# Performance work log

Hardware: AMD Instinct MI355X
Metric: run time of the kernel (lower is better)

Reference implementation:

```python
import jax, jax.numpy as jnp
import numpy as np

N_NODES = 50000
N_EDGES = 800000
IN_F, HID, OUT_F = 256, 128, 64
ATTN_SLOPE = 0.2   # DGL GATConv negative_slope default
ACT_SLOPE = 0.01   # nn.LeakyReLU default


def setup_inputs() -> dict:
    key = jax.random.key(0)
    ks = jax.random.split(key, 7)
    x = jax.random.normal(ks[0], (N_NODES, IN_F), dtype=jnp.float32)
    src = jax.random.randint(ks[1], (N_EDGES,), 0, N_NODES, dtype=jnp.int32)
    dst = jax.random.randint(ks[2], (N_EDGES,), 0, N_NODES, dtype=jnp.int32)
    W_gat = jax.random.normal(ks[3], (IN_F, HID), dtype=jnp.float32) * (1.0 / np.sqrt(IN_F))
    attn_l = jax.random.normal(ks[4], (HID,), dtype=jnp.float32) * 0.1
    attn_r = jax.random.normal(ks[5], (HID,), dtype=jnp.float32) * 0.1
    bias_gat = jnp.zeros((HID,), dtype=jnp.float32)
    W_lin = jax.random.normal(ks[6], (OUT_F, HID), dtype=jnp.float32) * (1.0 / np.sqrt(HID))
    return {"x": x, "src": src, "dst": dst, "W_gat": W_gat, "attn_l": attn_l,
            "attn_r": attn_r, "bias_gat": bias_gat, "W_lin": W_lin}


def reference(x, src, dst, W_gat, attn_l, attn_r, bias_gat, W_lin):
    N = x.shape[0]
    # GATConv (num_heads=1): linear projection then additive attention
    feat = x @ W_gat                         # [N, HID]
    el = feat @ attn_l                        # [N]  (sum(feat * a_l, -1))
    er = feat @ attn_r                        # [N]
    # per-edge logits, leaky_relu(0.2)
    e = jax.nn.leaky_relu(el[src] + er[dst], negative_slope=ATTN_SLOPE)  # [E]
    # segment softmax over edges grouped by destination node
    e_max = jax.ops.segment_max(e, dst, num_segments=N)  # [N] (-inf for isolated)
    alpha = jnp.exp(e - e_max[dst])                      # [E]
    denom = jax.ops.segment_sum(alpha, dst, num_segments=N)
    a = alpha / denom[dst]                               # [E]
    # scatter-weighted aggregation of source features
    msg = a[:, None] * feat[src]                         # [E, HID]
    agg = jax.ops.segment_sum(msg, dst, num_segments=N) + bias_gat  # [N, HID]
    # outer wrapper: LeakyReLU(0.01), squeeze (head dim already gone), linear no bias
    gene = jax.nn.leaky_relu(agg, negative_slope=ACT_SLOPE)
    return gene @ W_lin.T                                # [N, OUT_F]
```

## Files before the change

kernel.cpp:

```cpp
#include <hip/hip_runtime.h>
#include <hip/hip_bf16.h>


#define NNODES 50000
#define NEDGES 800000
#define IN_F   256
#define HID    128
#define OUTF   64

#define PA_EPT   12
#define PA_EDGES (256 * PA_EPT)
#define PA_NB    ((NEDGES + PA_EDGES - 1) / PA_EDGES)
#define NBKT     ((NNODES + 255) / 256)
#define BCAP     5120
#define GB       ((NNODES / 16 + 7) / 8)

typedef unsigned short u16;
typedef unsigned long long u64;
typedef __bf16 bf16x8 __attribute__((ext_vector_type(8)));
typedef float  f32x4  __attribute__((ext_vector_type(4)));

__device__ __forceinline__ u16 f2b(float f) {
    union { float f; unsigned u; } v; v.f = f;
    unsigned u = v.u;
    return (u16)((u + 0x7fffu + ((u >> 16) & 1u)) >> 16);
}
__device__ __forceinline__ float b2f_lo(unsigned v) {
    union { unsigned u; float f; } c; c.u = (v & 0xffffu) << 16; return c.f;
}
__device__ __forceinline__ float b2f_hi(unsigned v) {
    union { unsigned u; float f; } c; c.u = v & 0xffff0000u; return c.f;
}
__device__ __forceinline__ float lrelu02_exp(float t) {
    t = t > 0.f ? t : 0.2f * t;
    return __expf(t);
}

__global__ __launch_bounds__(256) void pack0(const float* __restrict__ Wg,
                                             const float* __restrict__ Wl,
                                             u16* __restrict__ pWg,
                                             u16* __restrict__ pWl,
                                             int* __restrict__ bcnt) {
    int blk = blockIdx.x, tid = threadIdx.x;
    if (blk < 16) {
        int t = blk * 256 + tid;
        int lane = t & 63, tile = t >> 6;
        int nt = tile & 7, kt = tile >> 3;
        int col = lane & 15, quad = lane >> 4;
        int krow = kt * 32 + quad * 8;
        int ncol = nt * 16 + col;
#pragma unroll
        for (int j = 0; j < 8; j++) pWg[t * 8 + j] = f2b(Wg[(krow + j) * HID + ncol]);
    } else if (blk < 20) {
        int t = (blk - 16) * 256 + tid;
        int lane = t & 63, tile = t >> 6;
        int nt = tile & 3, kt = tile >> 2;
        int col = lane & 15, quad = lane >> 4;
        int o  = nt * 16 + col;
        int k0 = kt * 32 + quad * 8;
#pragma unroll
        for (int j = 0; j < 8; j++) pWl[t * 8 + j] = f2b(Wl[o * HID + k0 + j]);
    } else {
        if (tid < NBKT) bcnt[tid] = 0;
    }
}

__global__ __launch_bounds__(256) void k_mega(
        const float* __restrict__ x, const u16* __restrict__ pWg,
        const float* __restrict__ al_, const float* __restrict__ ar_,
        unsigned* __restrict__ feat2, float* __restrict__ el, float* __restrict__ er,
        const int* __restrict__ src, const int* __restrict__ dst,
        int* __restrict__ bcnt, u64* __restrict__ pairs) {
    __shared__ char smem[35840];
    int blk = blockIdx.x, tid = threadIdx.x;

    if (blk < GB) {
        int wave = tid >> 6, lane = tid & 63;
        int strip0 = blk * 8 + wave * 2;
        if (strip0 >= NNODES / 16) return;
        bool two = (strip0 + 1 < NNODES / 16);
        int mA = strip0 * 16, mB = mA + 16;
        int col = lane & 15, quad = lane >> 4;

        f32x4 accA[8] = {}, accB[8] = {};
        const float* xrA = x + (size_t)(mA + col) * IN_F + quad * 8;
        const float* xrB = x + (size_t)(mB + col) * IN_F + quad * 8;
#pragma unroll
        for (int kt = 0; kt < 8; kt++) {
            f32x4 a0 = *reinterpret_cast<const f32x4*>(xrA + kt * 32);
            f32x4 a1 = *reinterpret_cast<const f32x4*>(xrA + kt * 32 + 4);
            f32x4 b0 = {}, b1 = {};
            if (two) {
                b0 = *reinterpret_cast<const f32x4*>(xrB + kt * 32);
                b1 = *reinterpret_cast<const f32x4*>(xrB + kt * 32 + 4);
            }
            bf16x8 avA, avB;
#pragma unroll
            for (int j = 0; j < 4; j++) {
                avA[j] = (__bf16)a0[j]; avA[4 + j] = (__bf16)a1[j];
                avB[j] = (__bf16)b0[j]; avB[4 + j] = (__bf16)b1[j];
            }
#pragma unroll
            for (int nt = 0; nt < 8; nt++) {
                bf16x8 b = *reinterpret_cast<const bf16x8*>(pWg + ((kt * 8 + nt) * 64 + lane) * 8);
                accA[nt] = __builtin_amdgcn_mfma_f32_16x16x32_bf16(avA, b, accA[nt], 0, 0, 0);
                accB[nt] = __builtin_amdgcn_mfma_f32_16x16x32_bf16(avB, b, accB[nt], 0, 0, 0);
            }
        }
        for (int ss = 0; ss < 2; ss++) {
            if (ss == 1 && !two) break;
            f32x4* acc = ss ? accB : accA;
            int m0 = ss ? mB : mA;
            float pl[4] = {0, 0, 0, 0}, pr[4] = {0, 0, 0, 0};
#pragma unroll
            for (int nt = 0; nt < 8; nt++) {
                float alv = al_[nt * 16 + col], arv = ar_[nt * 16 + col];
#pragma unroll
                for (int reg = 0; reg < 4; reg++) {
                    pl[reg] += acc[nt][reg] * alv;
                    pr[reg] += acc[nt][reg] * arv;
                }
            }
#pragma unroll
            for (int m = 1; m < 16; m <<= 1)
#pragma unroll
                for (int reg = 0; reg < 4; reg++) {
                    pl[reg] += __shfl_xor(pl[reg], m, 64);
                    pr[reg] += __shfl_xor(pr[reg], m, 64);
                }
            if (col == 0) {
#pragma unroll
                for (int reg = 0; reg < 4; reg++) {
                    el[m0 + quad * 4 + reg] = pl[reg];
                    er[m0 + quad * 4 + reg] = pr[reg];
                }
            }
#pragma unroll
            for (int nt = 0; nt < 8; nt++)
#pragma unroll
                for (int reg = 0; reg < 4; reg++) {
                    u16* fp = (u16*)feat2;
                    fp[(size_t)(m0 + quad * 4 + reg) * HID + nt * 16 + col] = f2b(acc[nt][reg]);
                }
        }
        return;
    }

    int* hist    = (int*)smem;
    int* binbase = hist + 256;
    int* gbase   = binbase + 256;
    int* fill    = gbase + 256;
    int* stmp    = fill + 256;
    u64* spair   = (u64*)(smem + 8192);
    unsigned char* sbin = (unsigned char*)(smem + 8192 + 24576);

    int e0 = (blk - GB) * PA_EDGES;
    int cnt = NEDGES - e0; if (cnt > PA_EDGES) cnt = PA_EDGES;

    hist[tid] = 0; fill[tid] = 0;
    __syncthreads();

    int es[PA_EPT], ed[PA_EPT];
#pragma unroll
    for (int j = 0; j < PA_EPT; j++) {
        int idx = e0 + j * 256 + tid;
        if (idx < NEDGES) {
            es[j] = src[idx];
            ed[j] = dst[idx];
            atomicAdd(&hist[ed[j] >> 8], 1);
        } else ed[j] = -1;
    }
    __syncthreads();

    stmp[tid] = (tid < NBKT) ? hist[tid] : 0;
    __syncthreads();
#pragma unroll
    for (int ofs = 1; ofs < 256; ofs <<= 1) {
        int u = (tid >= ofs) ? stmp[tid - ofs] : 0;
        __syncthreads();
        stmp[tid] += u;
        __syncthreads();
    }
    if (tid < NBKT) {
        binbase[tid] = stmp[tid] - hist[tid];
        if (hist[tid] > 0)
            gbase[tid] = tid * BCAP + atomicAdd(&bcnt[tid], hist[tid]);
    }
    __syncthreads();

#pragma unroll
    for (int j = 0; j < PA_EPT; j++) {
        if (ed[j] >= 0) {
            int b = ed[j] >> 8;
            int r = atomicAdd(&fill[b], 1);
            int loc = binbase[b] + r;
            spair[loc] = ((u64)(unsigned)ed[j] << 32) | (unsigned)es[j];
            sbin[loc] = (unsigned char)b;
        }
    }
    __syncthreads();

    for (int i = tid; i < cnt; i += 256) {
        int b = sbin[i];
        pairs[gbase[b] + (i - binbase[b])] = spair[i];
    }
}

__global__ __launch_bounds__(512) void k_fine(const u64* __restrict__ pairs,
                                              const int* __restrict__ bcnt,
                                              const float* __restrict__ el,
                                              const float* __restrict__ er,
                                              int* __restrict__ rowptr,
                                              int* __restrict__ esrc,
                                              float* __restrict__ ew,
                                              float* __restrict__ den) {
    __shared__ int sbc[256];
    __shared__ int nh[256];
    __shared__ int wsum[256];
    __shared__ int cur[256];
    __shared__ float dls[256];
    __shared__ float erl[256];

    int b = blockIdx.x, tid = threadIdx.x;
    int nb = b << 8;
    int nn = NNODES - nb; if (nn > 256) nn = 256;

    if (tid < 256) sbc[tid] = (tid < NBKT) ? bcnt[tid] : 0;
    __syncthreads();
#pragma unroll
    for (int ofs = 1; ofs < 256; ofs <<= 1) {
        int u = 0;
        if (tid < 256 && tid >= ofs) u = sbc[tid - ofs];
        __syncthreads();
        if (tid < 256) sbc[tid] += u;
        __syncthreads();
    }
    int cntb = bcnt[b];
    int base = sbc[b] - cntb;
    const u64* reg = pairs + (size_t)b * BCAP;

    if (tid < 256) {
        nh[tid] = 0;
        dls[tid] = 0.f;
        erl[tid] = (tid < nn) ? er[nb + tid] : 0.f;
    }
    __syncthreads();
    for (int i = tid; i < cntb; i += 512) {
        int d = (int)(unsigned)(reg[i] >> 32);
        atomicAdd(&nh[d - nb], 1);
    }
    __syncthreads();

    int c = (tid < 256) ? nh[tid] : 0;
    if (tid < 256) wsum[tid] = c;
    __syncthreads();
#pragma unroll
    for (int ofs = 1; ofs < 256; ofs <<= 1) {
        int u = 0;
        if (tid < 256 && tid >= ofs) u = wsum[tid - ofs];
        __syncthreads();
        if (tid < 256) wsum[tid] += u;
        __syncthreads();
    }
    if (tid < 256) {
        int o = base + wsum[tid] - c;
        cur[tid] = o;
        if (tid < nn) rowptr[nb + tid] = o;
    }
    if (b == NBKT - 1 && tid == 0) rowptr[NNODES] = NEDGES;
    __syncthreads();

    for (int i = tid; i < cntb; i += 512) {
        u64 p = reg[i];
        int s_ = (int)(unsigned)(p & 0xffffffffu);
        int d  = (int)(unsigned)(p >> 32);
        int dl = d - nb;
        float w = lrelu02_exp(el[s_] + erl[dl]);
        int pos = atomicAdd(&cur[dl], 1);
        esrc[pos] = s_;
        ew[pos] = w;
        atomicAdd(&dls[dl], w);
    }
    __syncthreads();
    if (tid < nn) den[nb + tid] = dls[tid];
}

__global__ __launch_bounds__(256) void k_aggout(const int* __restrict__ rowptr,
                                                const int* __restrict__ esrc,
                                                const float* __restrict__ ew,
                                                const float* __restrict__ den,
                                                const unsigned* __restrict__ feat2,
                                                const float* __restrict__ bias,
                                                const u16* __restrict__ pWl,
                                                float* __restrict__ out) {
    __shared__ unsigned sg[16 * 68];
    int wave = threadIdx.x >> 6, lane = threadIdx.x & 63;
    int m0 = blockIdx.x * 16;
    float bl = bias[lane * 2 + 0], bh = bias[lane * 2 + 1];

    for (int i = 0; i < 4; i++) {
        int r = wave * 4 + i;
        int n = m0 + r;
        int beg = rowptr[n], end = rowptr[n + 1];

        float p0 = 0.f, p1 = 0.f, q0 = 0.f, q1 = 0.f;
        float r0 = 0.f, r1 = 0.f, t0 = 0.f, t1 = 0.f;
        float u0 = 0.f, u1 = 0.f, x0 = 0.f, x1 = 0.f;
        float y0 = 0.f, y1 = 0.f, z0 = 0.f, z1 = 0.f;
        int j = beg;
        for (; j + 8 <= end; j += 8) {
            int s0 = esrc[j],     s1 = esrc[j + 1], s2 = esrc[j + 2], s3 = esrc[j + 3];
            int s4 = esrc[j + 4], s5 = esrc[j + 5], s6 = esrc[j + 6], s7 = esrc[j + 7];
            unsigned v0 = feat2[(size_t)s0 * 64 + lane];
            unsigned v1 = feat2[(size_t)s1 * 64 + lane];
            unsigned v2 = feat2[(size_t)s2 * 64 + lane];
            unsigned v3 = feat2[(size_t)s3 * 64 + lane];
            unsigned v4 = feat2[(size_t)s4 * 64 + lane];
            unsigned v5 = feat2[(size_t)s5 * 64 + lane];
            unsigned v6 = feat2[(size_t)s6 * 64 + lane];
            unsigned v7 = feat2[(size_t)s7 * 64 + lane];
            float w0 = ew[j],     w1 = ew[j + 1], w2 = ew[j + 2], w3 = ew[j + 3];
            float w4 = ew[j + 4], w5 = ew[j + 5], w6 = ew[j + 6], w7 = ew[j + 7];
            p0 += w0 * b2f_lo(v0); p1 += w0 * b2f_hi(v0);
            q0 += w1 * b2f_lo(v1); q1 += w1 * b2f_hi(v1);
            r0 += w2 * b2f_lo(v2); r1 += w2 * b2f_hi(v2);
            t0 += w3 * b2f_lo(v3); t1 += w3 * b2f_hi(v3);
            u0 += w4 * b2f_lo(v4); u1 += w4 * b2f_hi(v4);
            x0 += w5 * b2f_lo(v5); x1 += w5 * b2f_hi(v5);
            y0 += w6 * b2f_lo(v6); y1 += w6 * b2f_hi(v6);
            z0 += w7 * b2f_lo(v7); z1 += w7 * b2f_hi(v7);
        }
        if (j + 4 <= end) {
            int s0 = esrc[j], s1 = esrc[j + 1], s2 = esrc[j + 2], s3 = esrc[j + 3];
            unsigned v0 = feat2[(size_t)s0 * 64 + lane];
            unsigned v1 = feat2[(size_t)s1 * 64 + lane];
            unsigned v2 = feat2[(size_t)s2 * 64 + lane];
            unsigned v3 = feat2[(size_t)s3 * 64 + lane];
            float w0 = ew[j], w1 = ew[j + 1], w2 = ew[j + 2], w3 = ew[j + 3];
            p0 += w0 * b2f_lo(v0); p1 += w0 * b2f_hi(v0);
            q0 += w1 * b2f_lo(v1); q1 += w1 * b2f_hi(v1);
            r0 += w2 * b2f_lo(v2); r1 += w2 * b2f_hi(v2);
            t0 += w3 * b2f_lo(v3); t1 += w3 * b2f_hi(v3);
            j += 4;
        }
        for (; j < end; j++) {
            int s = esrc[j];
            float w = ew[j];
            unsigned v = feat2[(size_t)s * 64 + lane];
            p0 += w * b2f_lo(v); p1 += w * b2f_hi(v);
        }
        float a0 = ((p0 + q0) + (r0 + t0)) + ((u0 + x0) + (y0 + z0));
        float a1 = ((p1 + q1) + (r1 + t1)) + ((u1 + x1) + (y1 + z1));

        float dn = den[n];
        float inv = dn > 0.f ? 1.f / dn : 0.f;
        float g0 = a0 * inv + bl;
        float g1 = a1 * inv + bh;
        g0 = g0 > 0.f ? g0 : 0.01f * g0;
        g1 = g1 > 0.f ? g1 : 0.01f * g1;
        sg[r * 68 + lane] = (unsigned)f2b(g0) | ((unsigned)f2b(g1) << 16);
    }
    __syncthreads();

    int col = lane & 15, quad = lane >> 4;
    int nt = wave;
    f32x4 acc = {};
#pragma unroll
    for (int kt = 0; kt < 4; kt++) {
        bf16x8 a = *reinterpret_cast<const bf16x8*>(&sg[col * 68 + kt * 16 + quad * 4]);
        bf16x8 bf = *reinterpret_cast<const bf16x8*>(pWl + ((kt * 4 + nt) * 64 + lane) * 8);
        acc = __builtin_amdgcn_mfma_f32_16x16x32_bf16(a, bf, acc, 0, 0, 0);
    }
#pragma unroll
    for (int reg = 0; reg < 4; reg++)
        out[(size_t)(m0 + quad * 4 + reg) * OUTF + nt * 16 + col] = acc[reg];
}

extern "C" void kernel_launch(void* const* d_in, const int* in_sizes, int n_in,
                              void* d_out, int out_size, void* d_ws, size_t ws_size,
                              hipStream_t stream) {
    const float* x      = (const float*)d_in[0];
    const int*   src    = (const int*)d_in[1];
    const int*   dst    = (const int*)d_in[2];
    const float* Wg     = (const float*)d_in[3];
    const float* attn_l = (const float*)d_in[4];
    const float* attn_r = (const float*)d_in[5];
    const float* bias   = (const float*)d_in[6];
    const float* Wl     = (const float*)d_in[7];
    float* out          = (float*)d_out;

    char* ws = (char*)d_ws;
    size_t off = 0;
    auto alloc = [&](size_t b) { size_t r = off; off += (b + 255) & ~(size_t)255; return r; };
    size_t pwgOff  = alloc((size_t)8 * 8 * 64 * 8 * 2);
    size_t pwlOff  = alloc((size_t)4 * 4 * 64 * 8 * 2);
    size_t featOff = alloc((size_t)NNODES * HID * 2);
    size_t elOff   = alloc((size_t)NNODES * 4);
    size_t erOff   = alloc((size_t)NNODES * 4);
    size_t denOff  = alloc((size_t)NNODES * 4);
    size_t rowOff  = alloc((size_t)(NNODES + 1) * 4);
    size_t esrcOff = alloc((size_t)NEDGES * 4);
    size_t ewOff   = alloc((size_t)NEDGES * 4);
    size_t pairOff = alloc((size_t)NBKT * BCAP * 8);
    size_t bcntOff = alloc((size_t)NBKT * 4);

    u16*      pWg   = (u16*)(ws + pwgOff);
    u16*      pWl   = (u16*)(ws + pwlOff);
    unsigned* feat2 = (unsigned*)(ws + featOff);
    float*    el    = (float*)(ws + elOff);
    float*    er    = (float*)(ws + erOff);
    float*    den   = (float*)(ws + denOff);
    int*      rowp  = (int*)(ws + rowOff);
    int*      esrc  = (int*)(ws + esrcOff);
    float*    ew    = (float*)(ws + ewOff);
    u64*      pairs = (u64*)(ws + pairOff);
    int*      bcnt  = (int*)(ws + bcntOff);

    pack0<<<21, 256, 0, stream>>>(Wg, Wl, pWg, pWl, bcnt);
    k_mega<<<GB + PA_NB, 256, 0, stream>>>(x, pWg, attn_l, attn_r, feat2, el, er,
                                           src, dst, bcnt, pairs);
    k_fine<<<NBKT, 512, 0, stream>>>(pairs, bcnt, el, er, rowp, esrc, ew, den);
    k_aggout<<<NNODES / 16, 256, 0, stream>>>(rowp, esrc, ew, den, feat2, bias,
                                              pWl, out);
}
```

Baseline: 176.4 us.

## Shrink k_mega per-block footprint: one strip per wave, smaller edge tiles, drop sbin

```diff
diff --git a/kernel.cpp b/kernel.cpp
--- a/kernel.cpp
+++ b/kernel.cpp
@@ -8,12 +8,13 @@
 #define HID    128
 #define OUTF   64
 
-#define PA_EPT   12
+#define PA_EPT   8
 #define PA_EDGES (256 * PA_EPT)
 #define PA_NB    ((NEDGES + PA_EDGES - 1) / PA_EDGES)
 #define NBKT     ((NNODES + 255) / 256)
 #define BCAP     5120
-#define GB       ((NNODES / 16 + 7) / 8)
+#define NSTRIP   (NNODES / 16)
+#define GB       ((NSTRIP + 3) / 4)
 
 typedef unsigned short u16;
 typedef unsigned long long u64;
@@ -65,84 +66,71 @@
     }
 }
 
-__global__ __launch_bounds__(256) void k_mega(
+__global__ __launch_bounds__(256, 5) void k_mega(
         const float* __restrict__ x, const u16* __restrict__ pWg,
         const float* __restrict__ al_, const float* __restrict__ ar_,
         unsigned* __restrict__ feat2, float* __restrict__ el, float* __restrict__ er,
         const int* __restrict__ src, const int* __restrict__ dst,
         int* __restrict__ bcnt, u64* __restrict__ pairs) {
-    __shared__ char smem[35840];
+    __shared__ u64 smemU[21504 / 8];
+    char* smem = (char*)smemU;
     int blk = blockIdx.x, tid = threadIdx.x;
 
     if (blk < GB) {
         int wave = tid >> 6, lane = tid & 63;
-        int strip0 = blk * 8 + wave * 2;
-        if (strip0 >= NNODES / 16) return;
-        bool two = (strip0 + 1 < NNODES / 16);
-        int mA = strip0 * 16, mB = mA + 16;
+        int strip = blk * 4 + wave;
+        if (strip >= NSTRIP) return;
+        int m0 = strip * 16;
         int col = lane & 15, quad = lane >> 4;
 
-        f32x4 accA[8] = {}, accB[8] = {};
-        const float* xrA = x + (size_t)(mA + col) * IN_F + quad * 8;
-        const float* xrB = x + (size_t)(mB + col) * IN_F + quad * 8;
+        f32x4 acc[8] = {};
+        const float* xr = x + (size_t)(m0 + col) * IN_F + quad * 8;
 #pragma unroll
         for (int kt = 0; kt < 8; kt++) {
-            f32x4 a0 = *reinterpret_cast<const f32x4*>(xrA + kt * 32);
-            f32x4 a1 = *reinterpret_cast<const f32x4*>(xrA + kt * 32 + 4);
-            f32x4 b0 = {}, b1 = {};
-            if (two) {
-                b0 = *reinterpret_cast<const f32x4*>(xrB + kt * 32);
-                b1 = *reinterpret_cast<const f32x4*>(xrB + kt * 32 + 4);
-            }
-            bf16x8 avA, avB;
+            f32x4 a0 = *reinterpret_cast<const f32x4*>(xr + kt * 32);
+            f32x4 a1 = *reinterpret_cast<const f32x4*>(xr + kt * 32 + 4);
+            bf16x8 av;
 #pragma unroll
             for (int j = 0; j < 4; j++) {
-                avA[j] = (__bf16)a0[j]; avA[4 + j] = (__bf16)a1[j];
-                avB[j] = (__bf16)b0[j]; avB[4 + j] = (__bf16)b1[j];
+                av[j] = (__bf16)a0[j]; av[4 + j] = (__bf16)a1[j];
             }
 #pragma unroll
             for (int nt = 0; nt < 8; nt++) {
                 bf16x8 b = *reinterpret_cast<const bf16x8*>(pWg + ((kt * 8 + nt) * 64 + lane) * 8);
-                accA[nt] = __builtin_amdgcn_mfma_f32_16x16x32_bf16(avA, b, accA[nt], 0, 0, 0);
-                accB[nt] = __builtin_amdgcn_mfma_f32_16x16x32_bf16(avB, b, accB[nt], 0, 0, 0);
-            }
-        }
-        for (int ss = 0; ss < 2; ss++) {
-            if (ss == 1 && !two) break;
-            f32x4* acc = ss ? accB : accA;
-            int m0 = ss ? mB : mA;
-            float pl[4] = {0, 0, 0, 0}, pr[4] = {0, 0, 0, 0};
-#pragma unroll
-            for (int nt = 0; nt < 8; nt++) {
-                float alv = al_[nt * 16 + col], arv = ar_[nt * 16 + col];
-#pragma unroll
-                for (int reg = 0; reg < 4; reg++) {
-                    pl[reg] += acc[nt][reg] * alv;
-                    pr[reg] += acc[nt][reg] * arv;
-                }
-            }
-#pragma unroll
-            for (int m = 1; m < 16; m <<= 1)
-#pragma unroll
-                for (int reg = 0; reg < 4; reg++) {
-                    pl[reg] += __shfl_xor(pl[reg], m, 64);
-                    pr[reg] += __shfl_xor(pr[reg], m, 64);
-                }
-            if (col == 0) {
-#pragma unroll
-                for (int reg = 0; reg < 4; reg++) {
-                    el[m0 + quad * 4 + reg] = pl[reg];
-                    er[m0 + quad * 4 + reg] = pr[reg];
-                }
-            }
-#pragma unroll
-            for (int nt = 0; nt < 8; nt++)
-#pragma unroll
-                for (int reg = 0; reg < 4; reg++) {
-                    u16* fp = (u16*)feat2;
-                    fp[(size_t)(m0 + quad * 4 + reg) * HID + nt * 16 + col] = f2b(acc[nt][reg]);
-                }
-        }
+                acc[nt] = __builtin_amdgcn_mfma_f32_16x16x32_bf16(av, b, acc[nt], 0, 0, 0);
+            }
+        }
+        float pl[4] = {0, 0, 0, 0}, pr[4] = {0, 0, 0, 0};
+#pragma unroll
+        for (int nt = 0; nt < 8; nt++) {
+            float alv = al_[nt * 16 + col], arv = ar_[nt * 16 + col];
+#pragma unroll
+            for (int reg = 0; reg < 4; reg++) {
+                pl[reg] += acc[nt][reg] * alv;
+                pr[reg] += acc[nt][reg] * arv;
+            }
+        }
+#pragma unroll
+        for (int m = 1; m < 16; m <<= 1)
+#pragma unroll
+            for (int reg = 0; reg < 4; reg++) {
+                pl[reg] += __shfl_xor(pl[reg], m, 64);
+                pr[reg] += __shfl_xor(pr[reg], m, 64);
+            }
+        if (col == 0) {
+#pragma unroll
+            for (int reg = 0; reg < 4; reg++) {
+                el[m0 + quad * 4 + reg] = pl[reg];
+                er[m0 + quad * 4 + reg] = pr[reg];
+            }
+        }
+#pragma unroll
+        for (int nt = 0; nt < 8; nt++)
+#pragma unroll
+            for (int reg = 0; reg < 4; reg++) {
+                u16* fp = (u16*)feat2;
+                fp[(size_t)(m0 + quad * 4 + reg) * HID + nt * 16 + col] = f2b(acc[nt][reg]);
+            }
         return;
     }
 
@@ -151,8 +139,7 @@
     int* gbase   = binbase + 256;
     int* fill    = gbase + 256;
     int* stmp    = fill + 256;
-    u64* spair   = (u64*)(smem + 8192);
-    unsigned char* sbin = (unsigned char*)(smem + 8192 + 24576);
+    u64* spair   = (u64*)(smem + 5120);
 
     int e0 = (blk - GB) * PA_EDGES;
     int cnt = NEDGES - e0; if (cnt > PA_EDGES) cnt = PA_EDGES;
@@ -195,14 +182,14 @@
             int r = atomicAdd(&fill[b], 1);
             int loc = binbase[b] + r;
             spair[loc] = ((u64)(unsigned)ed[j] << 32) | (unsigned)es[j];
-            sbin[loc] = (unsigned char)b;
         }
     }
     __syncthreads();
 
     for (int i = tid; i < cnt; i += 256) {
-        int b = sbin[i];
-        pairs[gbase[b] + (i - binbase[b])] = spair[i];
+        u64 p = spair[i];
+        int b = (int)(p >> 40);
+        pairs[gbase[b] + (i - binbase[b])] = p;
     }
 }
 
```

Result: no change. 175.3 us (-0.6%).
